# Kernel tuning notes

Measured on AMD Instinct MI355X. Metric: run time of the kernel, lower is better.

## Reference

```python
import jax, jax.numpy as jnp
import numpy as np

NUM_HEADS = 12
N_TOKENS = 1

def setup_inputs() -> dict:
    key = jax.random.key(0)
    ks = jax.random.split(key, 13)
    D = 768
    s = 0.02
    return {
        "x": jax.random.normal(ks[0], (64, 1025, D), jnp.float32),
        "qW": jax.random.normal(ks[1], (D, D), jnp.float32) * s,
        "qb": jax.random.normal(ks[2], (D,), jnp.float32) * s,
        "kW": jax.random.normal(ks[3], (D, D), jnp.float32) * s,
        "kb": jax.random.normal(ks[4], (D,), jnp.float32) * s,
        "vW": jax.random.normal(ks[5], (D, D), jnp.float32) * s,
        "vb": jax.random.normal(ks[6], (D,), jnp.float32) * s,
        "w1W": jax.random.normal(ks[7], (NUM_HEADS, NUM_HEADS), jnp.float32) * 0.1,
        "w1b": jax.random.normal(ks[8], (NUM_HEADS,), jnp.float32) * 0.1,
        "w2W": jax.random.normal(ks[9], (NUM_HEADS, NUM_HEADS), jnp.float32) * 0.1,
        "w2b": jax.random.normal(ks[10], (NUM_HEADS,), jnp.float32) * 0.1,
        "projW": jax.random.normal(ks[11], (D, D), jnp.float32) * s,
        "projb": jax.random.normal(ks[12], (D,), jnp.float32) * s,
    }

def reference(x, qW, qb, kW, kb, vW, vb, w1W, w1b, w2W, w2b, projW, projb):
    B, N, C = x.shape  # C == embed_dim == 768
    H = NUM_HEADS
    d = C // H
    scale = d ** -0.5
    cls = x[:, :N_TOKENS]  # [B, n, C]
    # torch Linear: y = x @ W.T + b
    q = (cls @ qW.T + qb).reshape(B, N_TOKENS, H, d).transpose(0, 2, 1, 3) * scale  # [B,H,n,d]
    k = (x @ kW.T + kb).reshape(B, N, H, d).transpose(0, 2, 1, 3)  # [B,H,N,d]
    v = (x @ vW.T + vb).reshape(B, N, H, d).transpose(0, 2, 1, 3)  # [B,H,N,d]
    attn = jnp.einsum('bhqd,bhkd->bhqk', q, k)  # [B,H,n,N]
    # talking-heads pre-softmax: linear over head dim, added residually
    attn = attn + jnp.einsum('bhqk,gh->bgqk', attn, w1W) + w1b[None, :, None, None]
    attn = jax.nn.softmax(attn, axis=-1)
    # talking-heads post-softmax
    attn = attn + jnp.einsum('bhqk,gh->bgqk', attn, w2W) + w2b[None, :, None, None]
    out = jnp.einsum('bhqk,bhkd->bhqd', attn, v)  # [B,H,n,d]
    out = out.transpose(0, 2, 1, 3).reshape(B, N_TOKENS, C)
    return out @ projW.T + projb
```

## Files before the change

kernel.cpp:

```cpp
#include <hip/hip_runtime.h>

#define B 64
#define N 1025
#define NPAD 1028
#define C 768
#define H 12
#define HD 64

__device__ __forceinline__ float wave_reduce_add(float v) {
    #pragma unroll
    for (int m = 1; m < 64; m <<= 1) v += __shfl_xor(v, m, 64);
    return v;
}

__global__ __launch_bounds__(256) void k_qproj(const float* __restrict__ x,
                                               const float* __restrict__ qW,
                                               const float* __restrict__ qb,
                                               float* __restrict__ qout) {
    __shared__ float cls[4 * C];
    int bt = blockIdx.x, ct = blockIdx.y, tid = threadIdx.x;
    for (int i = tid; i < 768; i += 256) {
        int bl = i / 192, c4 = i % 192;
        ((float4*)cls)[i] = ((const float4*)(x + (size_t)(bt * 4 + bl) * N * C))[c4];
    }
    __syncthreads();
    int w = tid >> 6, lane = tid & 63;
    int b = bt * 4 + w;
    const float* clsrow = &cls[w * C];
    for (int cl = 0; cl < 16; ++cl) {
        int c = ct * 16 + cl;
        const float4* wr = (const float4*)(qW + (size_t)c * C + lane * 12);
        const float4* xr = (const float4*)(clsrow + lane * 12);
        float acc = 0.f;
        #pragma unroll
        for (int s = 0; s < 3; ++s) {
            float4 a = wr[s], v = xr[s];
            acc += a.x * v.x + a.y * v.y + a.z * v.z + a.w * v.w;
        }
        acc = wave_reduce_add(acc);
        if (lane == 0) qout[b * C + c] = 0.125f * (acc + qb[c]);
    }
}

__global__ __launch_bounds__(256) void k_qk(const float* __restrict__ q,
                                            const float* __restrict__ kW,
                                            const float* __restrict__ kb,
                                            float* __restrict__ qk,
                                            float* __restrict__ qkb) {
    int bt = blockIdx.x, h = blockIdx.y, tid = threadIdx.x;
    if (tid < 192) {
        float4 acc[4] = {};
        #pragma unroll 4
        for (int i = 0; i < HD; ++i) {
            int row = h * HD + i;
            float4 kv = *(const float4*)(kW + (size_t)row * C + tid * 4);
            #pragma unroll
            for (int bl = 0; bl < 4; ++bl) {
                float qv = q[(bt * 4 + bl) * C + row];
                acc[bl].x += qv * kv.x; acc[bl].y += qv * kv.y;
                acc[bl].z += qv * kv.z; acc[bl].w += qv * kv.w;
            }
        }
        #pragma unroll
        for (int bl = 0; bl < 4; ++bl) {
            int b = bt * 4 + bl;
            *(float4*)(qk + ((size_t)b * H + h) * C + tid * 4) = acc[bl];
        }
    }
    int w = tid >> 6, lane = tid & 63;
    int b = bt * 4 + w;
    float v = q[b * C + h * HD + lane] * kb[h * HD + lane];
    v = wave_reduce_add(v);
    if (lane == 0) qkb[b * H + h] = v;
}

__global__ __launch_bounds__(256) void k_scores(const float* __restrict__ x,
                                                const float* __restrict__ qk,
                                                float* __restrict__ sc) {
    __shared__ float qs[12 * C];
    int tile = blockIdx.x, b = blockIdx.y, tid = threadIdx.x;
    const float4* qksrc = (const float4*)(qk + (size_t)b * H * C);
    for (int i = tid; i < 2304; i += 256) ((float4*)qs)[i] = qksrc[i];
    __syncthreads();
    int w = tid >> 6, lane = tid & 63;
    int c16 = lane & 15, r = lane >> 4;
    int rowbase = tile * 64 + w * 16 + r * 4;
    const float* xb = x + (size_t)b * N * C;
    float acc[4][12] = {};
    for (int cc = 0; cc < C; cc += 128) {
        int c0 = cc + c16 * 4, c1 = c0 + 64;
        float4 xv0[4], xv1[4];
        #pragma unroll
        for (int j = 0; j < 4; ++j) {
            int row = rowbase + j;
            const float* xr = xb + (size_t)row * C;
            xv0[j] = (row < N) ? *(const float4*)(xr + c0) : make_float4(0.f,0.f,0.f,0.f);
            xv1[j] = (row < N) ? *(const float4*)(xr + c1) : make_float4(0.f,0.f,0.f,0.f);
        }
        #pragma unroll
        for (int h = 0; h < 12; ++h) {
            float4 q0 = *(const float4*)(qs + h * C + c0);
            float4 q1 = *(const float4*)(qs + h * C + c1);
            #pragma unroll
            for (int j = 0; j < 4; ++j) {
                acc[j][h] += xv0[j].x * q0.x + xv0[j].y * q0.y +
                             xv0[j].z * q0.z + xv0[j].w * q0.w;
                acc[j][h] += xv1[j].x * q1.x + xv1[j].y * q1.y +
                             xv1[j].z * q1.z + xv1[j].w * q1.w;
            }
        }
    }
    #pragma unroll
    for (int j = 0; j < 4; ++j)
        #pragma unroll
        for (int h = 0; h < 12; ++h) {
            float v = acc[j][h];
            v += __shfl_xor(v, 1); v += __shfl_xor(v, 2);
            v += __shfl_xor(v, 4); v += __shfl_xor(v, 8);
            acc[j][h] = v;
        }
    if (c16 == 0) {
        #pragma unroll
        for (int j = 0; j < 4; ++j) {
            int row = rowbase + j;
            if (row < N) {
                #pragma unroll
                for (int h = 0; h < 12; ++h)
                    sc[((size_t)b * H + h) * NPAD + row] = acc[j][h];
            }
        }
    }
}

__global__ __launch_bounds__(256) void k_mix1(float* __restrict__ sc,
                                              const float* __restrict__ qkbias,
                                              const float* __restrict__ w1W,
                                              const float* __restrict__ w1b,
                                              float* __restrict__ mstat,
                                              float* __restrict__ sstat) {
    __shared__ float w1s[144], w1bs[12], qbs[12];
    __shared__ float red[4][12];
    __shared__ float mg[12];
    int kk = blockIdx.x, b = blockIdx.y, tid = threadIdx.x;
    int nn = (kk == 7) ? 129 : 128;
    int n = kk * 128 + tid;
    if (tid < 144) w1s[tid] = w1W[tid];
    if (tid < 12)  { w1bs[tid] = w1b[tid]; qbs[tid] = qkbias[b * 12 + tid]; }
    __syncthreads();
    bool act = tid < nn;
    float o[12];
    if (act) {
        float s_[12];
        #pragma unroll
        for (int h = 0; h < 12; ++h)
            s_[h] = sc[((size_t)b * H + h) * NPAD + n] + qbs[h];
        #pragma unroll
        for (int g = 0; g < 12; ++g) {
            float a = s_[g] + w1bs[g];
            #pragma unroll
            for (int h = 0; h < 12; ++h) a += w1s[g * 12 + h] * s_[h];
            o[g] = a;
        }
        #pragma unroll
        for (int g = 0; g < 12; ++g)
            sc[((size_t)b * H + g) * NPAD + n] = o[g];
    } else {
        #pragma unroll
        for (int g = 0; g < 12; ++g) o[g] = -3e38f;
    }
    int w = tid >> 6, lane = tid & 63;
    #pragma unroll
    for (int g = 0; g < 12; ++g) {
        float v = o[g];
        #pragma unroll
        for (int m = 1; m < 64; m <<= 1) v = fmaxf(v, __shfl_xor(v, m, 64));
        if (lane == 0) red[w][g] = v;
    }
    __syncthreads();
    if (tid < 12)
        mg[tid] = fmaxf(fmaxf(red[0][tid], red[1][tid]),
                        fmaxf(red[2][tid], red[3][tid]));
    __syncthreads();
    #pragma unroll
    for (int g = 0; g < 12; ++g) {
        float e = act ? __expf(o[g] - mg[g]) : 0.f;
        e = wave_reduce_add(e);
        if (lane == 0) red[w][g] = e;
    }
    __syncthreads();
    if (tid < 12) {
        mstat[((size_t)b * 8 + kk) * 12 + tid] = mg[tid];
        sstat[((size_t)b * 8 + kk) * 12 + tid] =
            red[0][tid] + red[1][tid] + red[2][tid] + red[3][tid];
    }
}

#define FMA4(d, s, xv) { d.x += (s) * xv.x; d.y += (s) * xv.y; d.z += (s) * xv.z; d.w += (s) * xv.w; }
__global__ __launch_bounds__(192) void k_ysum(const float* __restrict__ x,
                                              const float* __restrict__ sc,
                                              const float* __restrict__ mstat,
                                              const float* __restrict__ sstat,
                                              const float* __restrict__ w2W,
                                              const float* __restrict__ w2b,
                                              float* __restrict__ yp) {
    __shared__ float as_[129 * 12];
    __shared__ float w2s[144], w2bs[12], msh[12], ish[12];
    int k = blockIdx.x, b = blockIdx.y, tid = threadIdx.x;
    int nlo = k * 128, nn = (k == 7) ? 129 : 128;
    if (tid < 144) w2s[tid] = w2W[tid];
    if (tid < 12) {
        w2bs[tid] = w2b[tid];
        float m = -3e38f, mv[8];
        #pragma unroll
        for (int kk = 0; kk < 8; ++kk) {
            mv[kk] = mstat[((size_t)b * 8 + kk) * 12 + tid];
            m = fmaxf(m, mv[kk]);
        }
        float S = 0.f;
        #pragma unroll
        for (int kk = 0; kk < 8; ++kk)
            S += sstat[((size_t)b * 8 + kk) * 12 + tid] * __expf(mv[kk] - m);
        msh[tid] = m; ish[tid] = 1.f / S;
    }
    __syncthreads();
    if (tid < nn) {
        int n = nlo + tid;
        float p[12];
        #pragma unroll
        for (int h = 0; h < 12; ++h)
            p[h] = __expf(sc[((size_t)b * H + h) * NPAD + n] - msh[h]) * ish[h];
        #pragma unroll
        for (int g = 0; g < 12; ++g) {
            float a = p[g] + w2bs[g];
            #pragma unroll
            for (int h = 0; h < 12; ++h) a += w2s[g * 12 + h] * p[h];
            as_[tid * 12 + g] = a;
        }
    }
    __syncthreads();
    const float* xb = x + ((size_t)b * N + nlo) * C + tid * 4;
    float4 acc[12] = {};
    int n = 0;
    for (; n + 4 <= nn; n += 4) {
        float4 xv[4];
        #pragma unroll
        for (int u = 0; u < 4; ++u)
            xv[u] = *(const float4*)(xb + (size_t)(n + u) * C);
        #pragma unroll
        for (int u = 0; u < 4; ++u) {
            const float4* ar = (const float4*)(as_ + (n + u) * 12);
            float4 a0 = ar[0], a1 = ar[1], a2 = ar[2];
            FMA4(acc[0], a0.x, xv[u]); FMA4(acc[1], a0.y, xv[u]); FMA4(acc[2], a0.z, xv[u]); FMA4(acc[3], a0.w, xv[u]);
            FMA4(acc[4], a1.x, xv[u]); FMA4(acc[5], a1.y, xv[u]); FMA4(acc[6], a1.z, xv[u]); FMA4(acc[7], a1.w, xv[u]);
            FMA4(acc[8], a2.x, xv[u]); FMA4(acc[9], a2.y, xv[u]); FMA4(acc[10], a2.z, xv[u]); FMA4(acc[11], a2.w, xv[u]);
        }
    }
    for (; n < nn; ++n) {
        float4 xv = *(const float4*)(xb + (size_t)n * C);
        const float4* ar = (const float4*)(as_ + n * 12);
        float4 a0 = ar[0], a1 = ar[1], a2 = ar[2];
        FMA4(acc[0], a0.x, xv); FMA4(acc[1], a0.y, xv); FMA4(acc[2], a0.z, xv); FMA4(acc[3], a0.w, xv);
        FMA4(acc[4], a1.x, xv); FMA4(acc[5], a1.y, xv); FMA4(acc[6], a1.z, xv); FMA4(acc[7], a1.w, xv);
        FMA4(acc[8], a2.x, xv); FMA4(acc[9], a2.y, xv); FMA4(acc[10], a2.z, xv); FMA4(acc[11], a2.w, xv);
    }
    #pragma unroll
    for (int h = 0; h < 12; ++h)
        *(float4*)(yp + (((size_t)k * B + b) * H + h) * C + tid * 4) = acc[h];
}

__global__ __launch_bounds__(256) void k_zproj(const float* __restrict__ yp,
                                               const float* __restrict__ vW,
                                               const float* __restrict__ vb,
                                               const float* __restrict__ w2W,
                                               const float* __restrict__ w2b,
                                               float* __restrict__ z) {
    __shared__ float ys[4 * C];
    int bt = blockIdx.x, h = blockIdx.y, tid = threadIdx.x;
    for (int i = tid; i < 768; i += 256) {
        int bl = i / 192, c4 = i % 192;
        int b = bt * 4 + bl;
        float4 s = make_float4(0.f, 0.f, 0.f, 0.f);
        #pragma unroll
        for (int k = 0; k < 8; ++k) {
            float4 v = ((const float4*)(yp + (((size_t)k * B + b) * H + h) * C))[c4];
            s.x += v.x; s.y += v.y; s.z += v.z; s.w += v.w;
        }
        ((float4*)ys)[i] = s;
    }
    __syncthreads();
    float sv = 1.f + 1025.f * w2b[h];
    #pragma unroll
    for (int j = 0; j < 12; ++j) sv += w2W[h * 12 + j];
    int w = tid >> 6, lane = tid & 63;
    int b = bt * 4 + w;
    const float* yrow = &ys[w * C];
    for (int cl = 0; cl < 64; ++cl) {
        int c = h * 64 + cl;
        const float4* wr = (const float4*)(vW + (size_t)c * C + lane * 12);
        const float4* yr = (const float4*)(yrow + lane * 12);
        float acc = 0.f;
        #pragma unroll
        for (int s = 0; s < 3; ++s) {
            float4 a = wr[s], v = yr[s];
            acc += a.x * v.x + a.y * v.y + a.z * v.z + a.w * v.w;
        }
        acc = wave_reduce_add(acc);
        if (lane == 0) z[b * C + c] = acc + vb[c] * sv;
    }
}

__global__ __launch_bounds__(256) void k_out(const float* __restrict__ z,
                                             const float* __restrict__ pW,
                                             const float* __restrict__ pb,
                                             float* __restrict__ out) {
    __shared__ float zs[4 * C];
    int bt = blockIdx.x, ct = blockIdx.y, tid = threadIdx.x;
    for (int i = tid; i < 768; i += 256)
        ((float4*)zs)[i] = ((const float4*)(z + (size_t)bt * 4 * C))[i];
    __syncthreads();
    int w = tid >> 6, lane = tid & 63;
    int b = bt * 4 + w;
    for (int cl = 0; cl < 16; ++cl) {
        int c = ct * 16 + cl;
        const float4* wr = (const float4*)(pW + (size_t)c * C + lane * 12);
        const float4* zr = (const float4*)(zs + w * C + lane * 12);
        float acc = 0.f;
        #pragma unroll
        for (int s = 0; s < 3; ++s) {
            float4 a = wr[s], v = zr[s];
            acc += a.x * v.x + a.y * v.y + a.z * v.z + a.w * v.w;
        }
        acc = wave_reduce_add(acc);
        if (lane == 0) out[b * C + c] = acc + pb[c];
    }
}

extern "C" void kernel_launch(void* const* d_in, const int* in_sizes, int n_in,
                              void* d_out, int out_size, void* d_ws, size_t ws_size,
                              hipStream_t stream) {
    const float* x    = (const float*)d_in[0];
    const float* qW   = (const float*)d_in[1];
    const float* qb   = (const float*)d_in[2];
    const float* kW   = (const float*)d_in[3];
    const float* kb   = (const float*)d_in[4];
    const float* vW   = (const float*)d_in[5];
    const float* vb   = (const float*)d_in[6];
    const float* w1W  = (const float*)d_in[7];
    const float* w1b  = (const float*)d_in[8];
    const float* w2W  = (const float*)d_in[9];
    const float* w2b  = (const float*)d_in[10];
    const float* pW   = (const float*)d_in[11];
    const float* pb   = (const float*)d_in[12];
    float* out = (float*)d_out;

    float* ws    = (float*)d_ws;
    float* qk    = ws + 0;
    float* qkb   = ws + 589824;
    float* q     = ws + 590592;
    float* sc    = ws + 639744;
    float* yp    = ws + 1429248;
    float* z     = ws + 6147840;
    float* mstat = ws + 6196992;
    float* sstat = ws + 6203136;

    k_qproj <<<dim3(16, 48), 256, 0, stream>>>(x, qW, qb, q);
    k_qk    <<<dim3(16, 12), 256, 0, stream>>>(q, kW, kb, qk, qkb);
    k_scores<<<dim3(17, 64), 256, 0, stream>>>(x, qk, sc);
    k_mix1  <<<dim3(8, 64), 256, 0, stream>>>(sc, qkb, w1W, w1b, mstat, sstat);
    k_ysum  <<<dim3(8, 64), 192, 0, stream>>>(x, sc, mstat, sstat, w2W, w2b, yp);
    k_zproj <<<dim3(16, 12), 256, 0, stream>>>(yp, vW, vb, w2W, w2b, z);
    k_out   <<<dim3(16, 48), 256, 0, stream>>>(z, pW, pb, out);
}
```

Before: 458.9 us.

## Fuse scores, softmax exp and value accumulation into one chunked kernel

Merges the q-projection with the qk kernel, and fuses score computation, the pre-softmax head mix, the exponential and the x-weighted accumulation into one kernel per 64-row chunk. Scores stay in shared memory instead of a global round trip, so x is read twice per chunk from cache rather than in separate passes. It drops max subtraction and relies on post-softmax mixing being linear, deferring normalization to a combine kernel that sums partial exp-weighted sums across chunks. This removes the separate stats pass, but the unnormalized exp risks overflow for large logits and adds a larger partial-sum buffer. k_zproj is also re-gridded across more blocks.

Result: slower. 471.6 us (+2.8%).

```diff
diff --git a/kernel.cpp b/kernel.cpp
--- a/kernel.cpp
+++ b/kernel.cpp
@@ -2,10 +2,10 @@
 
 #define B 64
 #define N 1025
-#define NPAD 1028
 #define C 768
 #define H 12
 #define HD 64
+#define NCH 16
 
 __device__ __forceinline__ float wave_reduce_add(float v) {
     #pragma unroll
@@ -13,23 +13,28 @@
     return v;
 }
 
-__global__ __launch_bounds__(256) void k_qproj(const float* __restrict__ x,
-                                               const float* __restrict__ qW,
-                                               const float* __restrict__ qb,
-                                               float* __restrict__ qout) {
-    __shared__ float cls[4 * C];
-    int bt = blockIdx.x, ct = blockIdx.y, tid = threadIdx.x;
+#define FMA4(d, s, xv) { d.x += (s) * xv.x; d.y += (s) * xv.y; d.z += (s) * xv.z; d.w += (s) * xv.w; }
+
+__global__ __launch_bounds__(256) void k_qkf(const float* __restrict__ x,
+                                             const float* __restrict__ qW,
+                                             const float* __restrict__ qb,
+                                             const float* __restrict__ kW,
+                                             const float* __restrict__ kb,
+                                             float* __restrict__ qk,
+                                             float* __restrict__ qkb) {
+    __shared__ __attribute__((aligned(16))) float cls[4 * C];
+    __shared__ float qv[4 * 64];
+    int bt = blockIdx.x, h = blockIdx.y, tid = threadIdx.x;
     for (int i = tid; i < 768; i += 256) {
         int bl = i / 192, c4 = i % 192;
         ((float4*)cls)[i] = ((const float4*)(x + (size_t)(bt * 4 + bl) * N * C))[c4];
     }
     __syncthreads();
     int w = tid >> 6, lane = tid & 63;
-    int b = bt * 4 + w;
     const float* clsrow = &cls[w * C];
-    for (int cl = 0; cl < 16; ++cl) {
-        int c = ct * 16 + cl;
-        const float4* wr = (const float4*)(qW + (size_t)c * C + lane * 12);
+    for (int i = 0; i < 64; ++i) {
+        int row = h * 64 + i;
+        const float4* wr = (const float4*)(qW + (size_t)row * C + lane * 12);
         const float4* xr = (const float4*)(clsrow + lane * 12);
         float acc = 0.f;
         #pragma unroll
@@ -38,254 +43,200 @@
             acc += a.x * v.x + a.y * v.y + a.z * v.z + a.w * v.w;
         }
         acc = wave_reduce_add(acc);
-        if (lane == 0) qout[b * C + c] = 0.125f * (acc + qb[c]);
-    }
-}
-
-__global__ __launch_bounds__(256) void k_qk(const float* __restrict__ q,
-                                            const float* __restrict__ kW,
-                                            const float* __restrict__ kb,
-                                            float* __restrict__ qk,
-                                            float* __restrict__ qkb) {
-    int bt = blockIdx.x, h = blockIdx.y, tid = threadIdx.x;
+        if (lane == 0) qv[w * 64 + i] = 0.125f * (acc + qb[row]);
+    }
+    __syncthreads();
     if (tid < 192) {
         float4 acc[4] = {};
-        #pragma unroll 4
-        for (int i = 0; i < HD; ++i) {
-            int row = h * HD + i;
-            float4 kv = *(const float4*)(kW + (size_t)row * C + tid * 4);
+        for (int i = 0; i < 64; ++i) {
+            float4 kv = *(const float4*)(kW + (size_t)(h * 64 + i) * C + tid * 4);
             #pragma unroll
             for (int bl = 0; bl < 4; ++bl) {
-                float qv = q[(bt * 4 + bl) * C + row];
-                acc[bl].x += qv * kv.x; acc[bl].y += qv * kv.y;
-                acc[bl].z += qv * kv.z; acc[bl].w += qv * kv.w;
-            }
-        }
-        #pragma unroll
-        for (int bl = 0; bl < 4; ++bl) {
-            int b = bt * 4 + bl;
-            *(float4*)(qk + ((size_t)b * H + h) * C + tid * 4) = acc[bl];
-        }
-    }
-    int w = tid >> 6, lane = tid & 63;
-    int b = bt * 4 + w;
-    float v = q[b * C + h * HD + lane] * kb[h * HD + lane];
-    v = wave_reduce_add(v);
-    if (lane == 0) qkb[b * H + h] = v;
-}
-
-__global__ __launch_bounds__(256) void k_scores(const float* __restrict__ x,
-                                                const float* __restrict__ qk,
-                                                float* __restrict__ sc) {
-    __shared__ float qs[12 * C];
-    int tile = blockIdx.x, b = blockIdx.y, tid = threadIdx.x;
+                float qq = qv[bl * 64 + i];
+                FMA4(acc[bl], qq, kv);
+            }
+        }
+        #pragma unroll
+        for (int bl = 0; bl < 4; ++bl)
+            *(float4*)(qk + ((size_t)(bt * 4 + bl) * H + h) * C + tid * 4) = acc[bl];
+    }
+    float vv = qv[w * 64 + lane] * kb[h * 64 + lane];
+    vv = wave_reduce_add(vv);
+    if (lane == 0) qkb[(bt * 4 + w) * H + h] = vv;
+}
+
+__global__ __launch_bounds__(256) void k_fused(const float* __restrict__ x,
+                                               const float* __restrict__ qk,
+                                               const float* __restrict__ qkb,
+                                               const float* __restrict__ w1W,
+                                               const float* __restrict__ w1b,
+                                               float* __restrict__ Ep,
+                                               float* __restrict__ Xp,
+                                               float* __restrict__ Sp) {
+    __shared__ __attribute__((aligned(16))) float qs[12 * C];
+    __shared__ __attribute__((aligned(16))) float et[66 * 12];
+    __shared__ float w1s[144], w1bs[12], qbs[12];
+    __shared__ float sred[4][12];
+    int k = blockIdx.x, b = blockIdx.y, tid = threadIdx.x;
+    int nlo = k * 64, nn = (k == NCH - 1) ? 65 : 64;
+    int rmax = nlo + nn;
     const float4* qksrc = (const float4*)(qk + (size_t)b * H * C);
     for (int i = tid; i < 2304; i += 256) ((float4*)qs)[i] = qksrc[i];
-    __syncthreads();
+    if (tid < 144) w1s[tid] = w1W[tid];
+    if (tid < 12)  { w1bs[tid] = w1b[tid]; qbs[tid] = qkb[b * 12 + tid]; }
+    __syncthreads();
+
     int w = tid >> 6, lane = tid & 63;
     int c16 = lane & 15, r = lane >> 4;
-    int rowbase = tile * 64 + w * 16 + r * 4;
     const float* xb = x + (size_t)b * N * C;
-    float acc[4][12] = {};
-    for (int cc = 0; cc < C; cc += 128) {
-        int c0 = cc + c16 * 4, c1 = c0 + 64;
-        float4 xv0[4], xv1[4];
-        #pragma unroll
-        for (int j = 0; j < 4; ++j) {
-            int row = rowbase + j;
-            const float* xr = xb + (size_t)row * C;
-            xv0[j] = (row < N) ? *(const float4*)(xr + c0) : make_float4(0.f,0.f,0.f,0.f);
-            xv1[j] = (row < N) ? *(const float4*)(xr + c1) : make_float4(0.f,0.f,0.f,0.f);
-        }
-        #pragma unroll
-        for (int h = 0; h < 12; ++h) {
-            float4 q0 = *(const float4*)(qs + h * C + c0);
-            float4 q1 = *(const float4*)(qs + h * C + c1);
+    for (int p = 0; p * 64 < nn; ++p) {
+        int rowbase = nlo + p * 64 + w * 16 + r * 4;
+        float acc[4][12] = {};
+        for (int cc = 0; cc < C; cc += 128) {
+            int c0 = cc + c16 * 4, c1 = c0 + 64;
+            float4 xv0[4], xv1[4];
             #pragma unroll
             for (int j = 0; j < 4; ++j) {
-                acc[j][h] += xv0[j].x * q0.x + xv0[j].y * q0.y +
-                             xv0[j].z * q0.z + xv0[j].w * q0.w;
-                acc[j][h] += xv1[j].x * q1.x + xv1[j].y * q1.y +
-                             xv1[j].z * q1.z + xv1[j].w * q1.w;
-            }
-        }
-    }
-    #pragma unroll
-    for (int j = 0; j < 4; ++j)
-        #pragma unroll
-        for (int h = 0; h < 12; ++h) {
-            float v = acc[j][h];
-            v += __shfl_xor(v, 1); v += __shfl_xor(v, 2);
-            v += __shfl_xor(v, 4); v += __shfl_xor(v, 8);
-            acc[j][h] = v;
-        }
-    if (c16 == 0) {
-        #pragma unroll
-        for (int j = 0; j < 4; ++j) {
-            int row = rowbase + j;
-            if (row < N) {
+                int row = rowbase + j;
+                const float* xr = xb + (size_t)row * C;
+                bool ok = row < rmax;
+                xv0[j] = ok ? *(const float4*)(xr + c0) : make_float4(0.f,0.f,0.f,0.f);
+                xv1[j] = ok ? *(const float4*)(xr + c1) : make_float4(0.f,0.f,0.f,0.f);
+            }
+            #pragma unroll
+            for (int h = 0; h < 12; ++h) {
+                float4 q0 = *(const float4*)(qs + h * C + c0);
+                float4 q1 = *(const float4*)(qs + h * C + c1);
                 #pragma unroll
-                for (int h = 0; h < 12; ++h)
-                    sc[((size_t)b * H + h) * NPAD + row] = acc[j][h];
-            }
-        }
-    }
-}
-
-__global__ __launch_bounds__(256) void k_mix1(float* __restrict__ sc,
-                                              const float* __restrict__ qkbias,
-                                              const float* __restrict__ w1W,
-                                              const float* __restrict__ w1b,
-                                              float* __restrict__ mstat,
-                                              float* __restrict__ sstat) {
-    __shared__ float w1s[144], w1bs[12], qbs[12];
-    __shared__ float red[4][12];
-    __shared__ float mg[12];
-    int kk = blockIdx.x, b = blockIdx.y, tid = threadIdx.x;
-    int nn = (kk == 7) ? 129 : 128;
-    int n = kk * 128 + tid;
-    if (tid < 144) w1s[tid] = w1W[tid];
-    if (tid < 12)  { w1bs[tid] = w1b[tid]; qbs[tid] = qkbias[b * 12 + tid]; }
-    __syncthreads();
+                for (int j = 0; j < 4; ++j) {
+                    acc[j][h] += xv0[j].x * q0.x + xv0[j].y * q0.y +
+                                 xv0[j].z * q0.z + xv0[j].w * q0.w;
+                    acc[j][h] += xv1[j].x * q1.x + xv1[j].y * q1.y +
+                                 xv1[j].z * q1.z + xv1[j].w * q1.w;
+                }
+            }
+        }
+        #pragma unroll
+        for (int j = 0; j < 4; ++j)
+            #pragma unroll
+            for (int h = 0; h < 12; ++h) {
+                float v = acc[j][h];
+                v += __shfl_xor(v, 1); v += __shfl_xor(v, 2);
+                v += __shfl_xor(v, 4); v += __shfl_xor(v, 8);
+                acc[j][h] = v;
+            }
+        if (c16 == 0) {
+            #pragma unroll
+            for (int j = 0; j < 4; ++j) {
+                int row = rowbase + j;
+                if (row < rmax) {
+                    #pragma unroll
+                    for (int h = 0; h < 12; ++h)
+                        et[(row - nlo) * 12 + h] = acc[j][h];
+                }
+            }
+        }
+    }
+    __syncthreads();
+
+    float e_[12];
     bool act = tid < nn;
-    float o[12];
     if (act) {
         float s_[12];
         #pragma unroll
-        for (int h = 0; h < 12; ++h)
-            s_[h] = sc[((size_t)b * H + h) * NPAD + n] + qbs[h];
+        for (int h = 0; h < 12; ++h) s_[h] = et[tid * 12 + h] + qbs[h];
         #pragma unroll
         for (int g = 0; g < 12; ++g) {
             float a = s_[g] + w1bs[g];
             #pragma unroll
             for (int h = 0; h < 12; ++h) a += w1s[g * 12 + h] * s_[h];
-            o[g] = a;
-        }
-        #pragma unroll
-        for (int g = 0; g < 12; ++g)
-            sc[((size_t)b * H + g) * NPAD + n] = o[g];
+            e_[g] = __expf(a);
+        }
+        #pragma unroll
+        for (int g = 0; g < 12; ++g) et[tid * 12 + g] = e_[g];
     } else {
         #pragma unroll
-        for (int g = 0; g < 12; ++g) o[g] = -3e38f;
-    }
-    int w = tid >> 6, lane = tid & 63;
+        for (int g = 0; g < 12; ++g) e_[g] = 0.f;
+    }
     #pragma unroll
     for (int g = 0; g < 12; ++g) {
-        float v = o[g];
-        #pragma unroll
-        for (int m = 1; m < 64; m <<= 1) v = fmaxf(v, __shfl_xor(v, m, 64));
-        if (lane == 0) red[w][g] = v;
+        float v = wave_reduce_add(e_[g]);
+        if (lane == 0) sred[w][g] = v;
     }
     __syncthreads();
     if (tid < 12)
-        mg[tid] = fmaxf(fmaxf(red[0][tid], red[1][tid]),
-                        fmaxf(red[2][tid], red[3][tid]));
-    __syncthreads();
-    #pragma unroll
-    for (int g = 0; g < 12; ++g) {
-        float e = act ? __expf(o[g] - mg[g]) : 0.f;
-        e = wave_reduce_add(e);
-        if (lane == 0) red[w][g] = e;
-    }
-    __syncthreads();
-    if (tid < 12) {
-        mstat[((size_t)b * 8 + kk) * 12 + tid] = mg[tid];
-        sstat[((size_t)b * 8 + kk) * 12 + tid] =
-            red[0][tid] + red[1][tid] + red[2][tid] + red[3][tid];
-    }
-}
-
-#define FMA4(d, s, xv) { d.x += (s) * xv.x; d.y += (s) * xv.y; d.z += (s) * xv.z; d.w += (s) * xv.w; }
-__global__ __launch_bounds__(192) void k_ysum(const float* __restrict__ x,
-                                              const float* __restrict__ sc,
-                                              const float* __restrict__ mstat,
-                                              const float* __restrict__ sstat,
-                                              const float* __restrict__ w2W,
-                                              const float* __restrict__ w2b,
-                                              float* __restrict__ yp) {
-    __shared__ float as_[129 * 12];
-    __shared__ float w2s[144], w2bs[12], msh[12], ish[12];
-    int k = blockIdx.x, b = blockIdx.y, tid = threadIdx.x;
-    int nlo = k * 128, nn = (k == 7) ? 129 : 128;
+        Sp[((size_t)b * NCH + k) * 12 + tid] =
+            sred[0][tid] + sred[1][tid] + sred[2][tid] + sred[3][tid];
+
+    if (tid < 192) {
+        const float* xr = x + ((size_t)b * N + nlo) * C + tid * 4;
+        float4 Eacc[12] = {};
+        float4 Xacc = make_float4(0.f, 0.f, 0.f, 0.f);
+        for (int n = 0; n < nn; ++n) {
+            float4 xv = *(const float4*)(xr + (size_t)n * C);
+            const float4* ar = (const float4*)(et + n * 12);
+            float4 a0 = ar[0], a1 = ar[1], a2 = ar[2];
+            FMA4(Eacc[0], a0.x, xv); FMA4(Eacc[1], a0.y, xv); FMA4(Eacc[2], a0.z, xv); FMA4(Eacc[3], a0.w, xv);
+            FMA4(Eacc[4], a1.x, xv); FMA4(Eacc[5], a1.y, xv); FMA4(Eacc[6], a1.z, xv); FMA4(Eacc[7], a1.w, xv);
+            FMA4(Eacc[8], a2.x, xv); FMA4(Eacc[9], a2.y, xv); FMA4(Eacc[10], a2.z, xv); FMA4(Eacc[11], a2.w, xv);
+            Xacc.x += xv.x; Xacc.y += xv.y; Xacc.z += xv.z; Xacc.w += xv.w;
+        }
+        #pragma unroll
+        for (int h = 0; h < 12; ++h)
+            *(float4*)(Ep + (((size_t)(k * B + b)) * H + h) * C + tid * 4) = Eacc[h];
+        *(float4*)(Xp + ((size_t)(k * B + b)) * C + tid * 4) = Xacc;
+    }
+}
+
+__global__ __launch_bounds__(192) void k_comby(const float* __restrict__ Ep,
+                                               const float* __restrict__ Xp,
+                                               const float* __restrict__ Sp,
+                                               const float* __restrict__ w2W,
+                                               const float* __restrict__ w2b,
+                                               float* __restrict__ y) {
+    __shared__ float is_[12], w2s[144], w2bs[12];
+    int cq = blockIdx.x, b = blockIdx.y, tid = threadIdx.x;
     if (tid < 144) w2s[tid] = w2W[tid];
     if (tid < 12) {
         w2bs[tid] = w2b[tid];
-        float m = -3e38f, mv[8];
-        #pragma unroll
-        for (int kk = 0; kk < 8; ++kk) {
-            mv[kk] = mstat[((size_t)b * 8 + kk) * 12 + tid];
-            m = fmaxf(m, mv[kk]);
-        }
         float S = 0.f;
         #pragma unroll
-        for (int kk = 0; kk < 8; ++kk)
-            S += sstat[((size_t)b * 8 + kk) * 12 + tid] * __expf(mv[kk] - m);
-        msh[tid] = m; ish[tid] = 1.f / S;
-    }
-    __syncthreads();
-    if (tid < nn) {
-        int n = nlo + tid;
-        float p[12];
-        #pragma unroll
-        for (int h = 0; h < 12; ++h)
-            p[h] = __expf(sc[((size_t)b * H + h) * NPAD + n] - msh[h]) * ish[h];
-        #pragma unroll
-        for (int g = 0; g < 12; ++g) {
-            float a = p[g] + w2bs[g];
-            #pragma unroll
-            for (int h = 0; h < 12; ++h) a += w2s[g * 12 + h] * p[h];
-            as_[tid * 12 + g] = a;
-        }
-    }
-    __syncthreads();
-    const float* xb = x + ((size_t)b * N + nlo) * C + tid * 4;
-    float4 acc[12] = {};
-    int n = 0;
-    for (; n + 4 <= nn; n += 4) {
-        float4 xv[4];
-        #pragma unroll
-        for (int u = 0; u < 4; ++u)
-            xv[u] = *(const float4*)(xb + (size_t)(n + u) * C);
-        #pragma unroll
-        for (int u = 0; u < 4; ++u) {
-            const float4* ar = (const float4*)(as_ + (n + u) * 12);
-            float4 a0 = ar[0], a1 = ar[1], a2 = ar[2];
-            FMA4(acc[0], a0.x, xv[u]); FMA4(acc[1], a0.y, xv[u]); FMA4(acc[2], a0.z, xv[u]); FMA4(acc[3], a0.w, xv[u]);
-            FMA4(acc[4], a1.x, xv[u]); FMA4(acc[5], a1.y, xv[u]); FMA4(acc[6], a1.z, xv[u]); FMA4(acc[7], a1.w, xv[u]);
-            FMA4(acc[8], a2.x, xv[u]); FMA4(acc[9], a2.y, xv[u]); FMA4(acc[10], a2.z, xv[u]); FMA4(acc[11], a2.w, xv[u]);
-        }
-    }
-    for (; n < nn; ++n) {
-        float4 xv = *(const float4*)(xb + (size_t)n * C);
-        const float4* ar = (const float4*)(as_ + n * 12);
-        float4 a0 = ar[0], a1 = ar[1], a2 = ar[2];
-        FMA4(acc[0], a0.x, xv); FMA4(acc[1], a0.y, xv); FMA4(acc[2], a0.z, xv); FMA4(acc[3], a0.w, xv);
-        FMA4(acc[4], a1.x, xv); FMA4(acc[5], a1.y, xv); FMA4(acc[6], a1.z, xv); FMA4(acc[7], a1.w, xv);
-        FMA4(acc[8], a2.x, xv); FMA4(acc[9], a2.y, xv); FMA4(acc[10], a2.z, xv); FMA4(acc[11], a2.w, xv);
-    }
-    #pragma unroll
-    for (int h = 0; h < 12; ++h)
-        *(float4*)(yp + (((size_t)k * B + b) * H + h) * C + tid * 4) = acc[h];
-}
-
-__global__ __launch_bounds__(256) void k_zproj(const float* __restrict__ yp,
+        for (int k = 0; k < NCH; ++k) S += Sp[((size_t)b * NCH + k) * 12 + tid];
+        is_[tid] = 1.f / S;
+    }
+    __syncthreads();
+    int c = cq * 192 + tid;
+    float Eh[12] = {};
+    float X = 0.f;
+    for (int k = 0; k < NCH; ++k) {
+        const float* base = Ep + ((size_t)(k * B + b)) * H * C + c;
+        #pragma unroll
+        for (int h = 0; h < 12; ++h) Eh[h] += base[(size_t)h * C];
+        X += Xp[((size_t)(k * B + b)) * C + c];
+    }
+    #pragma unroll
+    for (int h = 0; h < 12; ++h) Eh[h] *= is_[h];
+    #pragma unroll
+    for (int g = 0; g < 12; ++g) {
+        float yv = Eh[g] + w2bs[g] * X;
+        #pragma unroll
+        for (int h = 0; h < 12; ++h) yv += w2s[g * 12 + h] * Eh[h];
+        y[((size_t)b * H + g) * C + c] = yv;
+    }
+}
+
+__global__ __launch_bounds__(256) void k_zproj(const float* __restrict__ y,
                                                const float* __restrict__ vW,
                                                const float* __restrict__ vb,
                                                const float* __restrict__ w2W,
                                                const float* __restrict__ w2b,
                                                float* __restrict__ z) {
-    __shared__ float ys[4 * C];
-    int bt = blockIdx.x, h = blockIdx.y, tid = threadIdx.x;
+    __shared__ __attribute__((aligned(16))) float ys[4 * C];
+    int bt = blockIdx.x, ct = blockIdx.y, tid = threadIdx.x;
+    int h = ct >> 2;
     for (int i = tid; i < 768; i += 256) {
         int bl = i / 192, c4 = i % 192;
-        int b = bt * 4 + bl;
-        float4 s = make_float4(0.f, 0.f, 0.f, 0.f);
-        #pragma unroll
-        for (int k = 0; k < 8; ++k) {
-            float4 v = ((const float4*)(yp + (((size_t)k * B + b) * H + h) * C))[c4];
-            s.x += v.x; s.y += v.y; s.z += v.z; s.w += v.w;
-        }
-        ((float4*)ys)[i] = s;
+        ((float4*)ys)[i] = ((const float4*)(y + (((size_t)(bt * 4 + bl)) * H + h) * C))[c4];
     }
     __syncthreads();
     float sv = 1.f + 1025.f * w2b[h];
@@ -294,8 +245,8 @@
     int w = tid >> 6, lane = tid & 63;
     int b = bt * 4 + w;
     const float* yrow = &ys[w * C];
-    for (int cl = 0; cl < 64; ++cl) {
-        int c = h * 64 + cl;
+    for (int cl = 0; cl < 16; ++cl) {
+        int c = ct * 16 + cl;
         const float4* wr = (const float4*)(vW + (size_t)c * C + lane * 12);
         const float4* yr = (const float4*)(yrow + lane * 12);
         float acc = 0.f;
@@ -313,7 +264,7 @@
                                              const float* __restrict__ pW,
                                              const float* __restrict__ pb,
                                              float* __restrict__ out) {
-    __shared__ float zs[4 * C];
+    __shared__ __attribute__((aligned(16))) float zs[4 * C];
     int bt = blockIdx.x, ct = blockIdx.y, tid = threadIdx.x;
     for (int i = tid; i < 768; i += 256)
         ((float4*)zs)[i] = ((const float4*)(z + (size_t)bt * 4 * C))[i];
@@ -353,21 +304,18 @@
     const float* pb   = (const float*)d_in[12];
     float* out = (float*)d_out;
 
-    float* ws    = (float*)d_ws;
-    float* qk    = ws + 0;
-    float* qkb   = ws + 589824;
-    float* q     = ws + 590592;
-    float* sc    = ws + 639744;
-    float* yp    = ws + 1429248;
-    float* z     = ws + 6147840;
-    float* mstat = ws + 6196992;
-    float* sstat = ws + 6203136;
-
-    k_qproj <<<dim3(16, 48), 256, 0, stream>>>(x, qW, qb, q);
-    k_qk    <<<dim3(16, 12), 256, 0, stream>>>(q, kW, kb, qk, qkb);
-    k_scores<<<dim3(17, 64), 256, 0, stream>>>(x, qk, sc);
-    k_mix1  <<<dim3(8, 64), 256, 0, stream>>>(sc, qkb, w1W, w1b, mstat, sstat);
-    k_ysum  <<<dim3(8, 64), 192, 0, stream>>>(x, sc, mstat, sstat, w2W, w2b, yp);
-    k_zproj <<<dim3(16, 12), 256, 0, stream>>>(yp, vW, vb, w2W, w2b, z);
-    k_out   <<<dim3(16, 48), 256, 0, stream>>>(z, pW, pb, out);
-}
+    float* ws  = (float*)d_ws;
+    float* qk  = ws + 0;
+    float* qkb = ws + 589824;
+    float* Ep  = ws + 590592;
+    float* Xp  = ws + 10027776;
+    float* Sp  = ws + 10814208;
+    float* y   = ws + 10826496;
+    float* z   = ws + 11416320;
+
+    k_qkf  <<<dim3(16, 12), 256, 0, stream>>>(x, qW, qb, kW, kb, qk, qkb);
+    k_fused<<<dim3(NCH, 64), 256, 0, stream>>>(x, qk, qkb, w1W, w1b, Ep, Xp, Sp);
+    k_comby<<<dim3(4, 64), 192, 0, stream>>>(Ep, Xp, Sp, w2W, w2b, y);
+    k_zproj<<<dim3(16, 48), 256, 0, stream>>>(y, vW, vb, w2W, w2b, z);
+    k_out  <<<dim3(16, 48), 256, 0, stream>>>(z, pW, pb, out);
+}
```
